# Performance work log

Hardware: AMD Instinct MI355X
Metric: run time of the kernel (lower is better)

The kernel has to match this reference:

```python
import jax, jax.numpy as jnp
import numpy as np
from jax import lax

H = 1024        # hidden_size
V_IN = 32000    # input_size (source vocab)
V_OUT = 32000   # output_size (target vocab)
S = 128         # source sentence length
MAX_STEPS = 51  # decode loop bound (loop <= 50)
EOS = 2         # target_vocab['<eos>']


def _lstm_cell(x, h, c, W_ih, W_hh, b_ih, b_hh):
    # torch LSTMCell: gate order i, f, g, o
    gates = jnp.dot(W_ih, x) + b_ih + jnp.dot(W_hh, h) + b_hh  # [4H]
    i, f, g, o = jnp.split(gates, 4)
    i = jax.nn.sigmoid(i)
    f = jax.nn.sigmoid(f)
    g = jnp.tanh(g)
    o = jax.nn.sigmoid(o)
    c2 = f * c + i * g
    return o * jnp.tanh(c2), c2


def setup_inputs() -> dict:
    key = jax.random.key(0)
    ks = jax.random.split(key, 16)
    sc = 0.02
    p = {}
    p['src_ids'] = jax.random.randint(ks[0], (S,), 1, V_IN)
    emb_in = jax.random.normal(ks[1], (V_IN, H), jnp.float32) * sc
    p['embed_input'] = emb_in.at[0].set(0.0)  # padding_idx=0
    p['W_ih_e'] = jax.random.normal(ks[2], (4 * H, H), jnp.float32) * sc
    p['W_hh_e'] = jax.random.normal(ks[3], (4 * H, H), jnp.float32) * sc
    p['b_ih_e'] = jnp.zeros((4 * H,), jnp.float32)
    p['b_hh_e'] = jnp.zeros((4 * H,), jnp.float32)
    p['W_li'] = jax.random.normal(ks[4], (V_OUT, H), jnp.float32) * sc
    p['b_li'] = jnp.zeros((V_OUT,), jnp.float32)
    emb_t = jax.random.normal(ks[5], (V_OUT, H), jnp.float32) * sc
    p['embed_target'] = emb_t.at[0].set(0.0)  # padding_idx=0
    p['W_ih_d'] = jax.random.normal(ks[6], (4 * H, H), jnp.float32) * sc
    p['W_hh_d'] = jax.random.normal(ks[7], (4 * H, H), jnp.float32) * sc
    p['b_ih_d'] = jnp.zeros((4 * H,), jnp.float32)
    p['b_hh_d'] = jnp.zeros((4 * H,), jnp.float32)
    p['W_lt'] = jax.random.normal(ks[8], (V_OUT, H), jnp.float32) * sc
    p['b_lt'] = jnp.zeros((V_OUT,), jnp.float32)
    p['W_tl'] = jax.random.normal(ks[9], (H, 2 * H), jnp.float32) * sc
    p['b_tl'] = jnp.zeros((H,), jnp.float32)
    return p


def reference(src_ids, embed_input, W_ih_e, W_hh_e, b_ih_e, b_hh_e,
              W_li, b_li, embed_target, W_ih_d, W_hh_d, b_ih_d, b_hh_d,
              W_lt, b_lt, W_tl, b_tl):
    # ---- encoder: sequential LSTMCell over source tokens ----
    def enc_step(carry, tok):
        h, c = carry
        x = embed_input[tok]
        h2, c2 = _lstm_cell(x, h, c, W_ih_e, W_hh_e, b_ih_e, b_hh_e)
        return (h2, c2), h2

    h0 = jnp.zeros((H,), embed_input.dtype)
    (hs, cx), hs_all = lax.scan(enc_step, (h0, h0), src_ids)  # hs_all: [S,H]

    # first predicted word from final encoder state (argmax(softmax(z)) == argmax(z))
    wid0 = jnp.argmax(jnp.dot(W_li, hs) + b_li)
    tk0 = embed_target[wid0]
    ht, cx = _lstm_cell(tk0, hs, cx, W_ih_d, W_hh_d, b_ih_d, b_hh_d)

    # ---- greedy decode loop (fixed 51 steps, masked after <eos>) ----
    def dec_step(carry, _):
        wid, ht, cx, done = carry
        target_k = embed_target[wid]
        # dot-product attention over encoder states, softmax along source dim
        scores = jnp.dot(hs_all, ht)              # [S]
        a_t = jax.nn.softmax(scores)              # [S]
        d = jnp.dot(a_t, hs_all)                  # [H]
        concat = jnp.concatenate([d, ht])         # [2H]
        ht_new = jnp.tanh(jnp.dot(W_tl, concat) + b_tl)
        logits = jnp.dot(W_lt, ht_new) + b_lt     # [V_OUT]
        wid_new = jnp.argmax(logits)
        is_eos = wid_new == EOS
        out_tok = jnp.where(done | is_eos, -1, wid_new)  # -1 = not emitted
        ht2, cx2 = _lstm_cell(target_k, ht, cx, W_ih_d, W_hh_d, b_ih_d, b_hh_d)
        return (wid_new, ht2, cx2, done | is_eos), (out_tok, logits)

    done0 = wid0 == EOS
    _, (toks, logits) = lax.scan(dec_step, (wid0, ht, cx, done0), None, length=MAX_STEPS)
    return toks, logits  # toks: [51] emitted ids (-1 after eos), logits: [51, V_OUT]
```

## Files before the change

kernel.cpp:

```cpp
#include <hip/hip_runtime.h>
#include <float.h>
#include <math.h>

#define H      1024
#define SLEN   128
#define VOUT   32000
#define NSTEP  51
#define EOS_ID 2
#define NB     256
#define BT     1024
#define NWAVES 16
#define HROWS  4
#define LROWS  125
#define TOKS_OFF 51
#define QTAB_BYTES (LROWS*H)

typedef float fv4 __attribute__((ext_vector_type(4)));

struct Xch {
  unsigned long long h [2][H];
  unsigned long long ht[2][H];
  unsigned long long sc[2][SLEN];
  unsigned long long pv[2][NB];
};
__device__ Xch g_x;

__device__ __forceinline__ float wredsum(float v){
  v += __shfl_xor(v, 32, 64);
  v += __shfl_xor(v, 16, 64);
  v += __shfl_xor(v,  8, 64);
  v += __shfl_xor(v,  4, 64);
  v += __shfl_xor(v,  2, 64);
  v += __shfl_xor(v,  1, 64);
  return v;
}
__device__ __forceinline__ float wredmax(float v){
  v = fmaxf(v, __shfl_xor(v, 32, 64));
  v = fmaxf(v, __shfl_xor(v, 16, 64));
  v = fmaxf(v, __shfl_xor(v,  8, 64));
  v = fmaxf(v, __shfl_xor(v,  4, 64));
  v = fmaxf(v, __shfl_xor(v,  2, 64));
  v = fmaxf(v, __shfl_xor(v,  1, 64));
  return v;
}
__device__ __forceinline__ float sigm(float x){ return 1.0f/(1.0f+expf(-x)); }

__device__ __forceinline__ unsigned long long pollraw(const unsigned long long* p, unsigned tag){
  unsigned long long v = __hip_atomic_load(p, __ATOMIC_RELAXED, __HIP_MEMORY_SCOPE_AGENT);
  while((unsigned)(v & 0xffull) != tag){
    __builtin_amdgcn_s_sleep(1);
    v = __hip_atomic_load(p, __ATOMIC_RELAXED, __HIP_MEMORY_SCOPE_AGENT);
  }
  return v;
}
__device__ __forceinline__ float pollf(const unsigned long long* p, unsigned tag){
  return __uint_as_float((unsigned)(pollraw(p, tag) >> 32));
}
__device__ __forceinline__ void pubf(unsigned long long* p, float x, unsigned tag){
  __hip_atomic_store(p, (((unsigned long long)__float_as_uint(x))<<32) | (unsigned long long)tag,
                     __ATOMIC_RELAXED, __HIP_MEMORY_SCOPE_AGENT);
}
__device__ __forceinline__ void pubpv(unsigned long long* p, float v, int idx, unsigned tag){
  unsigned long long lo = (((unsigned long long)(unsigned)idx) << 8) | (unsigned long long)tag;
  __hip_atomic_store(p, (((unsigned long long)__float_as_uint(v))<<32) | lo,
                     __ATOMIC_RELAXED, __HIP_MEMORY_SCOPE_AGENT);
}

__device__ __forceinline__ float partdot(const float* __restrict__ a,
                                         const float* __restrict__ hp, int lane){
  const float4* a4 = (const float4*)a;
  const float4* h4 = (const float4*)hp;
  float s = 0.f;
#pragma unroll
  for(int k=0;k<4;k++){
    float4 x = a4[lane + 64*k];
    float4 y = h4[lane + 64*k];
    s = fmaf(x.x,y.x,s); s = fmaf(x.y,y.y,s);
    s = fmaf(x.z,y.z,s); s = fmaf(x.w,y.w,s);
  }
  return s;
}
__device__ __forceinline__ float partdot_nt(const float* __restrict__ a,
                                            const float* __restrict__ hp, int lane){
  const fv4* a4 = (const fv4*)a;
  const float4* h4 = (const float4*)hp;
  float s = 0.f;
#pragma unroll
  for(int k=0;k<4;k++){
    fv4 x = __builtin_nontemporal_load(a4 + lane + 64*k);
    float4 y = h4[lane + 64*k];
    s = fmaf(x.x,y.x,s); s = fmaf(x.y,y.y,s);
    s = fmaf(x.z,y.z,s); s = fmaf(x.w,y.w,s);
  }
  return s;
}

__device__ __forceinline__ float dotq(unsigned u, float4 hv, float acc){
  acc = fmaf((float)((int)(u<<24)>>24), hv.x, acc);
  acc = fmaf((float)((int)(u<<16)>>24), hv.y, acc);
  acc = fmaf((float)((int)(u<< 8)>>24), hv.z, acc);
  acc = fmaf((float)((int) u     >>24), hv.w, acc);
  return acc;
}

extern "C" __global__ void __launch_bounds__(BT)
nmt_kernel(const int* __restrict__ src_ids,
           const float* __restrict__ embed_input,
           const float* __restrict__ W_ih_e, const float* __restrict__ W_hh_e,
           const float* __restrict__ b_ih_e, const float* __restrict__ b_hh_e,
           const float* __restrict__ W_li,  const float* __restrict__ b_li,
           const float* __restrict__ embed_target,
           const float* __restrict__ W_ih_d, const float* __restrict__ W_hh_d,
           const float* __restrict__ b_ih_d, const float* __restrict__ b_hh_d,
           const float* __restrict__ W_lt,  const float* __restrict__ b_lt,
           const float* __restrict__ W_tl,  const float* __restrict__ b_tl,
           float* __restrict__ out)
{
  const int tid  = threadIdx.x;
  const int b    = blockIdx.x;
  const int w    = tid >> 6;
  const int lane = tid & 63;
  const int grow = (w>>2)*H + 4*b + (w&3);

  extern __shared__ __align__(16) char qmem[];
  uint4* qtab = (uint4*)qmem;

  __shared__ __align__(16) float hbuf[H];
  __shared__ __align__(16) float hsrow[H];
  __shared__ __align__(16) float htn_lds[H];
  __shared__ __align__(16) float xenc[SLEN][NWAVES];
  __shared__ __align__(16) float Mloc[HROWS][SLEN];
  __shared__ __align__(16) float sraw[SLEN];
  __shared__ __align__(16) float vloc[128];
  __shared__ __align__(16) float qrho[128];
  __shared__ __align__(16) float qinv[128];
  __shared__ __align__(16) float qbias[128];
  __shared__ int   rlist[128];
  __shared__ float gw4[4][4];
  __shared__ float c4[4];
  __shared__ float hn2[NWAVES];
  __shared__ float wred2[4];
  __shared__ float redv[NWAVES];
  __shared__ int   redi[NWAVES];
  __shared__ float gwhh_l[NWAVES];
  __shared__ int   wid_sh, done_sh;
  __shared__ float e_sh, rhomax_sh;
  __shared__ int   rcnt_sh;

#define PVCOMBINE(TAG) do{                                                     \
    if(w<4){                                                                   \
      unsigned long long v = pollraw(&g_x.pv[(TAG)&1][(w<<6)+lane], (TAG));    \
      float val = __uint_as_float((unsigned)(v>>32));                          \
      int   idx = (int)((unsigned)(v>>8) & 0xffffffu);                         \
      _Pragma("unroll")                                                        \
      for(int dd=32; dd>=1; dd>>=1){                                           \
        float ov=__shfl_xor(val,dd,64); int oi=__shfl_xor(idx,dd,64);          \
        if(ov>val || (ov==val && oi<idx)){ val=ov; idx=oi; }                   \
      }                                                                        \
      if(lane==0){ redv[w]=val; redi[w]=idx; }                                 \
    }                                                                          \
    __syncthreads();                                                           \
  }while(0)

  hbuf[tid] = 0.f;
  if(tid<4) c4[tid] = 0.f;
  __syncthreads();

  {
    const float4* wr = (const float4*)(W_ih_e + (size_t)grow*H);
    float4 w0=wr[lane], w1=wr[lane+64], w2=wr[lane+128], w3=wr[lane+192];
    const float bias = b_ih_e[grow] + b_hh_e[grow];
    for(int t=0;t<SLEN;t++){
      const float4* xr = (const float4*)(embed_input + (size_t)src_ids[t]*H);
      float4 x0=xr[lane], x1=xr[lane+64], x2=xr[lane+128], x3=xr[lane+192];
      float s;
      s = w0.x*x0.x;        s = fmaf(w0.y,x0.y,s); s = fmaf(w0.z,x0.z,s); s = fmaf(w0.w,x0.w,s);
      s = fmaf(w1.x,x1.x,s); s = fmaf(w1.y,x1.y,s); s = fmaf(w1.z,x1.z,s); s = fmaf(w1.w,x1.w,s);
      s = fmaf(w2.x,x2.x,s); s = fmaf(w2.y,x2.y,s); s = fmaf(w2.z,x2.z,s); s = fmaf(w2.w,x2.w,s);
      s = fmaf(w3.x,x3.x,s); s = fmaf(w3.y,x3.y,s); s = fmaf(w3.w,x3.w,s); s = fmaf(w3.z,x3.z,s);
      s = wredsum(s);
      if(lane==0) xenc[t][w] = s + bias;
    }
  }
  __syncthreads();

  for(int t=0;t<SLEN;t++){
    {
      float s = wredsum(partdot(W_hh_e + (size_t)grow*H, hbuf, lane)) + xenc[t][w];
      if(lane==0) gw4[w>>2][w&3] = s;
    }
    __syncthreads();
    if(tid<4){
      float gi=gw4[0][tid], gf=gw4[1][tid], gg=gw4[2][tid], go=gw4[3][tid];
      float ii=sigm(gi), ff=sigm(gf), g2=tanhf(gg), oo=sigm(go);
      float c2=fmaf(ff, c4[tid], ii*g2);
      c4[tid]=c2;
      pubf(&g_x.h[(t+1)&1][4*b+tid], oo*tanhf(c2), (unsigned)(t+1));
    }
    hbuf[tid] = pollf(&g_x.h[(t+1)&1][tid], (unsigned)(t+1));
    __syncthreads();
    if(b==t) hsrow[tid]=hbuf[tid];
    if(w<HROWS){
      float s2 = wredsum(partdot(W_tl + (size_t)(4*b+w)*2*H, hbuf, lane));
      if(lane==0) Mloc[w][t]=s2;
    }
  }
  __syncthreads();

  {
    const int rbase = b*LROWS;
#pragma unroll
    for(int t=0;t<8;t++){
      const int j = w + NWAVES*t;
      if(j < LROWS){
        const fv4* wr = (const fv4*)(W_lt + (size_t)(rbase+j)*H);
        fv4 g0=__builtin_nontemporal_load(wr+4*lane);
        fv4 g1=__builtin_nontemporal_load(wr+4*lane+1);
        fv4 g2=__builtin_nontemporal_load(wr+4*lane+2);
        fv4 g3=__builtin_nontemporal_load(wr+4*lane+3);
        float4 f0={g0.x,g0.y,g0.z,g0.w}, f1={g1.x,g1.y,g1.z,g1.w};
        float4 f2={g2.x,g2.y,g2.z,g2.w}, f3={g3.x,g3.y,g3.z,g3.w};
        float m;
        m = fmaxf(fabsf(f0.x),fabsf(f0.y)); m=fmaxf(m,fmaxf(fabsf(f0.z),fabsf(f0.w)));
        m = fmaxf(m,fmaxf(fabsf(f1.x),fabsf(f1.y))); m=fmaxf(m,fmaxf(fabsf(f1.z),fabsf(f1.w)));
        m = fmaxf(m,fmaxf(fabsf(f2.x),fabsf(f2.y))); m=fmaxf(m,fmaxf(fabsf(f2.z),fabsf(f2.w)));
        m = fmaxf(m,fmaxf(fabsf(f3.x),fabsf(f3.y))); m=fmaxf(m,fmaxf(fabsf(f3.z),fabsf(f3.w)));
        m = wredmax(m);
        const float s    = (m>1e-30f) ? 127.0f/m : 0.f;
        const float invs = (m>1e-30f) ? m*(1.0f/127.0f) : 0.f;
        float rsq = 0.f;
        unsigned pk[4];
        float4 ff[4] = {f0,f1,f2,f3};
#pragma unroll
        for(int u=0;u<4;u++){
          int q0=(int)rintf(ff[u].x*s), q1=(int)rintf(ff[u].y*s);
          int q2=(int)rintf(ff[u].z*s), q3=(int)rintf(ff[u].w*s);
          float d0=ff[u].x-(float)q0*invs, d1=ff[u].y-(float)q1*invs;
          float d2=ff[u].z-(float)q2*invs, d3=ff[u].w-(float)q3*invs;
          rsq=fmaf(d0,d0,rsq); rsq=fmaf(d1,d1,rsq);
          rsq=fmaf(d2,d2,rsq); rsq=fmaf(d3,d3,rsq);
          pk[u] = ((unsigned)(q0&255)) | ((unsigned)(q1&255)<<8)
                | ((unsigned)(q2&255)<<16) | ((unsigned)(q3&255)<<24);
        }
        uint4 qq; qq.x=pk[0]; qq.y=pk[1]; qq.z=pk[2]; qq.w=pk[3];
        qtab[j*64 + lane] = qq;
        rsq = wredsum(rsq);
        if(lane==0){
          qrho[j]  = sqrtf(rsq)*1.0002f + 1e-8f;
          qinv[j]  = invs;
          qbias[j] = b_lt[rbase+j];
        }
      }
    }
  }
  __syncthreads();
  {
    float rv = (tid<LROWS) ? qrho[tid] : 0.f;
    if(tid<128){
      float m = wredmax(rv);
      if(lane==0) wred2[w]=m;
    }
  }
  __syncthreads();
  if(tid==0) rhomax_sh = fmaxf(wred2[0], wred2[1]);

  {
    float bestv=-FLT_MAX; int besti=0;
    for(int j=w; j<LROWS; j+=NWAVES){
      const int r = b*LROWS + j;
      float s = wredsum(partdot_nt(W_li + (size_t)r*H, hbuf, lane));
      if(lane==0){
        float v = s + b_li[r];
        if(v>bestv){ bestv=v; besti=r; }
      }
    }
    if(lane==0){ redv[w]=bestv; redi[w]=besti; }
    __syncthreads();
    if(tid==0){
      float bv=redv[0]; int bi=redi[0];
      for(int i=1;i<NWAVES;i++)
        if(redv[i]>bv || (redv[i]==bv && redi[i]<bi)){ bv=redv[i]; bi=redi[i]; }
      pubpv(&g_x.pv[1][b], bv, bi, 1u);
    }
  }
  PVCOMBINE(1u);
  if(tid==0){
    float bv=redv[0]; int bi=redi[0];
    for(int i=1;i<4;i++)
      if(redv[i]>bv || (redv[i]==bv && redi[i]<bi)){ bv=redv[i]; bi=redi[i]; }
    wid_sh = bi;
    done_sh = (bi==EOS_ID) ? 1 : 0;
  }
  __syncthreads();

  {
    const float* tk = embed_target + (size_t)wid_sh*H;
    float s = partdot(W_ih_d + (size_t)grow*H, tk, lane)
            + partdot(W_hh_d + (size_t)grow*H, hbuf, lane);
    s = wredsum(s);
    if(lane==0) gw4[w>>2][w&3] = s + b_ih_d[grow] + b_hh_d[grow];
  }
  __syncthreads();
  if(tid<4){
    float gi=gw4[0][tid], gf=gw4[1][tid], gg=gw4[2][tid], go=gw4[3][tid];
    float ii=sigm(gi), ff=sigm(gf), g2=tanhf(gg), oo=sigm(go);
    float c2=fmaf(ff, c4[tid], ii*g2);
    c4[tid]=c2;
    pubf(&g_x.h[1][4*b+tid], oo*tanhf(c2), 129u);
  }
  hbuf[tid] = pollf(&g_x.h[1][tid], 129u);
  __syncthreads();
  if(b<SLEN && w==0){
    float s = wredsum(partdot(hsrow, hbuf, lane));
    if(lane==0) pubf(&g_x.sc[1][b], s, 1u);
  }
  {
    float s=wredsum(partdot(W_hh_d + (size_t)grow*H, hbuf, lane));
    if(lane==0) gwhh_l[w]=s;
  }
  __syncthreads();

  for(int k=0;k<NSTEP;k++){
    const unsigned htag = (unsigned)(130+k);
    const unsigned ttag = (unsigned)(k+1);
    if(k>0){
      PVCOMBINE((unsigned)(k+1));
      if(tid==0){
        float bv=redv[0]; int bi=redi[0];
        for(int i=1;i<4;i++)
          if(redv[i]>bv || (redv[i]==bv && redi[i]<bi)){ bv=redv[i]; bi=redi[i]; }
        int iseos=(bi==EOS_ID)?1:0;
        if(b==0) out[k-1]=(float)((done_sh|iseos)?-1:bi);
        done_sh |= iseos;
        wid_sh = bi;
      }
      __syncthreads();
    }
    if(tid<SLEN) sraw[tid] = pollf(&g_x.sc[(k+1)&1][tid], (unsigned)(k+1));
    __syncthreads();
    if(tid<SLEN){
      float m = wredmax(sraw[tid]);
      if(lane==0) wred2[w]=m;
    }
    __syncthreads();
    if(tid<SLEN){
      float mx=fmaxf(wred2[0],wred2[1]);
      float e=expf(sraw[tid]-mx);
      sraw[tid]=e;
      float z=wredsum(e);
      if(lane==0) wred2[2+w]=z;
    }
    __syncthreads();
    {
      const float* tk=embed_target + (size_t)wid_sh*H;
      float s=wredsum(partdot(W_ih_d + (size_t)grow*H, tk, lane));
      if(lane==0) gw4[w>>2][w&3] = s + gwhh_l[w] + b_ih_d[grow] + b_hh_d[grow];
    }
    if(w<HROWS){
      const int r=4*b+w;
      float invZ=1.f/(wred2[2]+wred2[3]);
      float att=fmaf(sraw[2*lane],Mloc[w][2*lane], sraw[2*lane+1]*Mloc[w][2*lane+1]);
      float s=partdot(W_tl + (size_t)r*2*H + H, hbuf, lane);
      float tot=wredsum(fmaf(att,invZ,s));
      if(lane==0) pubf(&g_x.ht[ttag&1][r], tanhf(tot + b_tl[r]), ttag);
    }
    __syncthreads();
    if(tid<4){
      float gi=gw4[0][tid], gf=gw4[1][tid], gg=gw4[2][tid], go=gw4[3][tid];
      float ii=sigm(gi), ff=sigm(gf), g2=tanhf(gg), oo=sigm(go);
      float c2=fmaf(ff, c4[tid], ii*g2);
      c4[tid]=c2;
      pubf(&g_x.h[htag&1][4*b+tid], oo*tanhf(c2), htag);
    }
    htn_lds[tid] = pollf(&g_x.ht[ttag&1][tid], ttag);
    hbuf[tid]    = pollf(&g_x.h [htag&1][tid], htag);
    __syncthreads();
    {
      float x = htn_lds[tid];
      float ss = wredsum(x*x);
      if(lane==0) hn2[w]=ss;
      if(tid==0) rcnt_sh=0;
    }
    __syncthreads();
    if(tid==0){
      float t2=0.f;
      for(int i=0;i<NWAVES;i++) t2+=hn2[i];
      float e = rhomax_sh * sqrtf(t2) * 1.0002f + 2e-3f;
      if(!(e>0.f && e<1e6f)) e=3.0e38f;
      e_sh = e;
    }
    {
      const float4* h4=(const float4*)htn_lds;
      float4 h0=h4[4*lane], h1=h4[4*lane+1], h2=h4[4*lane+2], h3=h4[4*lane+3];
#pragma unroll
      for(int t=0;t<8;t++){
        const int j=w+NWAVES*t;
        if(j<LROWS){
          uint4 q = qtab[j*64 + lane];
          float acc=0.f;
          acc=dotq(q.x,h0,acc); acc=dotq(q.y,h1,acc);
          acc=dotq(q.z,h2,acc); acc=dotq(q.w,h3,acc);
          acc=wredsum(acc);
          if(lane==0) vloc[j] = acc*qinv[j] + qbias[j];
        }
      }
    }
    __syncthreads();
    {
      const size_t obase = TOKS_OFF + (size_t)k*VOUT + (size_t)b*LROWS;
      if(tid<LROWS) out[obase+tid]=vloc[tid];
      float mv=(tid<LROWS)?vloc[tid]:-FLT_MAX;
      if(tid<128){
        float m=wredmax(mv);
        if(lane==0) wred2[w]=m;
      }
    }
    __syncthreads();
    {
      float thr = fmaxf(wred2[0],wred2[1]) - 2.0f*e_sh;
      if(tid<LROWS && vloc[tid]>=thr){
        int pos=atomicAdd(&rcnt_sh,1);
        rlist[pos]=tid;
      }
    }
    __syncthreads();
    {
      float bestv=-FLT_MAX; int besti=0x7fffffff;
      const int nr=rcnt_sh;
      for(int s2=w;s2<nr;s2+=NWAVES){
        const int r=b*LROWS+rlist[s2];
        float s=wredsum(partdot_nt(W_lt + (size_t)r*H, htn_lds, lane));
        if(lane==0){
          float f=s+qbias[rlist[s2]];
          if(f>bestv || (f==bestv && r<besti)){ bestv=f; besti=r; }
        }
      }
      if(lane==0){ redv[w]=bestv; redi[w]=besti; }
    }
    if(b<SLEN && w==0){
      float s=wredsum(partdot(hsrow, hbuf, lane));
      if(lane==0) pubf(&g_x.sc[(k+2)&1][b], s, (unsigned)(k+2));
    }
    {
      float s=wredsum(partdot(W_hh_d + (size_t)grow*H, hbuf, lane));
      if(lane==0) gwhh_l[w]=s;
    }
    __syncthreads();
    if(tid==0){
      float bv=redv[0]; int bi=redi[0];
      for(int i=1;i<NWAVES;i++)
        if(redv[i]>bv || (redv[i]==bv && redi[i]<bi)){ bv=redv[i]; bi=redi[i]; }
      pubpv(&g_x.pv[(k+2)&1][b], bv, bi, (unsigned)(k+2));
    }
  }

  if(b==0){
    PVCOMBINE((unsigned)(NSTEP+1));
    if(tid==0){
      float bv=redv[0]; int bi=redi[0];
      for(int i=1;i<4;i++)
        if(redv[i]>bv || (redv[i]==bv && redi[i]<bi)){ bv=redv[i]; bi=redi[i]; }
      int iseos=(bi==EOS_ID)?1:0;
      out[NSTEP-1]=(float)((done_sh|iseos)?-1:bi);
    }
  }
#undef PVCOMBINE
}

extern "C" void kernel_launch(void* const* d_in, const int* in_sizes, int n_in,
                              void* d_out, int out_size, void* d_ws, size_t ws_size,
                              hipStream_t stream) {
  const int*   src_ids      = (const int*)  d_in[0];
  const float* embed_input  = (const float*)d_in[1];
  const float* W_ih_e       = (const float*)d_in[2];
  const float* W_hh_e       = (const float*)d_in[3];
  const float* b_ih_e       = (const float*)d_in[4];
  const float* b_hh_e       = (const float*)d_in[5];
  const float* W_li         = (const float*)d_in[6];
  const float* b_li         = (const float*)d_in[7];
  const float* embed_target = (const float*)d_in[8];
  const float* W_ih_d       = (const float*)d_in[9];
  const float* W_hh_d       = (const float*)d_in[10];
  const float* b_ih_d       = (const float*)d_in[11];
  const float* b_hh_d       = (const float*)d_in[12];
  const float* W_lt         = (const float*)d_in[13];
  const float* b_lt         = (const float*)d_in[14];
  const float* W_tl         = (const float*)d_in[15];
  const float* b_tl         = (const float*)d_in[16];
  float*       out          = (float*)d_out;

  void* sptr = nullptr;
  (void)hipGetSymbolAddress(&sptr, HIP_SYMBOL(g_x));
  if(sptr) (void)hipMemsetAsync(sptr, 0, sizeof(Xch), stream);

  void* args[] = {
    (void*)&src_ids, (void*)&embed_input,
    (void*)&W_ih_e, (void*)&W_hh_e, (void*)&b_ih_e, (void*)&b_hh_e,
    (void*)&W_li, (void*)&b_li, (void*)&embed_target,
    (void*)&W_ih_d, (void*)&W_hh_d, (void*)&b_ih_d, (void*)&b_hh_d,
    (void*)&W_lt, (void*)&b_lt, (void*)&W_tl, (void*)&b_tl,
    (void*)&out
  };

  hipError_t err = hipLaunchCooperativeKernel((const void*)nmt_kernel,
                                              dim3(NB), dim3(BT), args,
                                              QTAB_BYTES, stream);
  if (err != hipSuccess) {
    nmt_kernel<<<dim3(NB), dim3(BT), QTAB_BYTES, stream>>>(
        src_ids, embed_input, W_ih_e, W_hh_e, b_ih_e, b_hh_e,
        W_li, b_li, embed_target, W_ih_d, W_hh_d, b_ih_d, b_hh_d,
        W_lt, b_lt, W_tl, b_tl, out);
  }
}
```

Baseline: 2.420 ms.

## Reorder decode step so argmax poll overlaps attention and h poll moves late

Reorders the per-step schedule of the persistent decode kernel. The attention/W_tl output projection is now computed before the cross-block argmax combine, and waves 4-7 poll the argmax partials so they do not collide with waves 0-3 doing attention. The hidden-state poll and the score/W_hh products move to the end of the step, after the vocab-logit pass, so the inter-block wait overlaps other work. The encoder input projection is also unrolled by two tokens to expose more memory parallelism. This adds extra barriers and changes the dependency order, so ordering mistakes could introduce stalls or races.

```diff
diff --git a/kernel.cpp b/kernel.cpp
--- a/kernel.cpp
+++ b/kernel.cpp
@@ -147,9 +147,9 @@
   __shared__ float e_sh, rhomax_sh;
   __shared__ int   rcnt_sh;
 
-#define PVCOMBINE(TAG) do{                                                     \
-    if(w<4){                                                                   \
-      unsigned long long v = pollraw(&g_x.pv[(TAG)&1][(w<<6)+lane], (TAG));    \
+#define PVPOLL47(TAG) do{                                                      \
+    if(w>=4 && w<8){                                                           \
+      unsigned long long v = pollraw(&g_x.pv[(TAG)&1][((w-4)<<6)+lane], (TAG));\
       float val = __uint_as_float((unsigned)(v>>32));                          \
       int   idx = (int)((unsigned)(v>>8) & 0xffffffu);                         \
       _Pragma("unroll")                                                        \
@@ -159,7 +159,6 @@
       }                                                                        \
       if(lane==0){ redv[w]=val; redi[w]=idx; }                                 \
     }                                                                          \
-    __syncthreads();                                                           \
   }while(0)
 
   hbuf[tid] = 0.f;
@@ -170,16 +169,22 @@
     const float4* wr = (const float4*)(W_ih_e + (size_t)grow*H);
     float4 w0=wr[lane], w1=wr[lane+64], w2=wr[lane+128], w3=wr[lane+192];
     const float bias = b_ih_e[grow] + b_hh_e[grow];
-    for(int t=0;t<SLEN;t++){
+    for(int t=0;t<SLEN;t+=2){
       const float4* xr = (const float4*)(embed_input + (size_t)src_ids[t]*H);
+      const float4* yr = (const float4*)(embed_input + (size_t)src_ids[t+1]*H);
       float4 x0=xr[lane], x1=xr[lane+64], x2=xr[lane+128], x3=xr[lane+192];
-      float s;
+      float4 y0=yr[lane], y1=yr[lane+64], y2=yr[lane+128], y3=yr[lane+192];
+      float s, u;
       s = w0.x*x0.x;        s = fmaf(w0.y,x0.y,s); s = fmaf(w0.z,x0.z,s); s = fmaf(w0.w,x0.w,s);
+      u = w0.x*y0.x;        u = fmaf(w0.y,y0.y,u); u = fmaf(w0.z,y0.z,u); u = fmaf(w0.w,y0.w,u);
       s = fmaf(w1.x,x1.x,s); s = fmaf(w1.y,x1.y,s); s = fmaf(w1.z,x1.z,s); s = fmaf(w1.w,x1.w,s);
+      u = fmaf(w1.x,y1.x,u); u = fmaf(w1.y,y1.y,u); u = fmaf(w1.z,y1.z,u); u = fmaf(w1.w,y1.w,u);
       s = fmaf(w2.x,x2.x,s); s = fmaf(w2.y,x2.y,s); s = fmaf(w2.z,x2.z,s); s = fmaf(w2.w,x2.w,s);
+      u = fmaf(w2.x,y2.x,u); u = fmaf(w2.y,y2.y,u); u = fmaf(w2.z,y2.z,u); u = fmaf(w2.w,y2.w,u);
       s = fmaf(w3.x,x3.x,s); s = fmaf(w3.y,x3.y,s); s = fmaf(w3.w,x3.w,s); s = fmaf(w3.z,x3.z,s);
-      s = wredsum(s);
-      if(lane==0) xenc[t][w] = s + bias;
+      u = fmaf(w3.x,y3.x,u); u = fmaf(w3.y,y3.y,u); u = fmaf(w3.w,y3.w,u); u = fmaf(w3.z,y3.z,u);
+      s = wredsum(s); u = wredsum(u);
+      if(lane==0){ xenc[t][w] = s + bias; xenc[t+1][w] = u + bias; }
     }
   }
   __syncthreads();
@@ -283,10 +288,12 @@
       pubpv(&g_x.pv[1][b], bv, bi, 1u);
     }
   }
-  PVCOMBINE(1u);
+  __syncthreads();
+  PVPOLL47(1u);
+  __syncthreads();
   if(tid==0){
-    float bv=redv[0]; int bi=redi[0];
-    for(int i=1;i<4;i++)
+    float bv=redv[4]; int bi=redi[4];
+    for(int i=5;i<8;i++)
       if(redv[i]>bv || (redv[i]==bv && redi[i]<bi)){ bv=redv[i]; bi=redi[i]; }
     wid_sh = bi;
     done_sh = (bi==EOS_ID) ? 1 : 0;
@@ -323,20 +330,7 @@
   for(int k=0;k<NSTEP;k++){
     const unsigned htag = (unsigned)(130+k);
     const unsigned ttag = (unsigned)(k+1);
-    if(k>0){
-      PVCOMBINE((unsigned)(k+1));
-      if(tid==0){
-        float bv=redv[0]; int bi=redi[0];
-        for(int i=1;i<4;i++)
-          if(redv[i]>bv || (redv[i]==bv && redi[i]<bi)){ bv=redv[i]; bi=redi[i]; }
-        int iseos=(bi==EOS_ID)?1:0;
-        if(b==0) out[k-1]=(float)((done_sh|iseos)?-1:bi);
-        done_sh |= iseos;
-        wid_sh = bi;
-      }
-      __syncthreads();
-    }
-    if(tid<SLEN) sraw[tid] = pollf(&g_x.sc[(k+1)&1][tid], (unsigned)(k+1));
+    if(tid<SLEN) sraw[tid] = pollf(&g_x.sc[ttag&1][tid], ttag);
     __syncthreads();
     if(tid<SLEN){
       float m = wredmax(sraw[tid]);
@@ -351,11 +345,6 @@
       if(lane==0) wred2[2+w]=z;
     }
     __syncthreads();
-    {
-      const float* tk=embed_target + (size_t)wid_sh*H;
-      float s=wredsum(partdot(W_ih_d + (size_t)grow*H, tk, lane));
-      if(lane==0) gw4[w>>2][w&3] = s + gwhh_l[w] + b_ih_d[grow] + b_hh_d[grow];
-    }
     if(w<HROWS){
       const int r=4*b+w;
       float invZ=1.f/(wred2[2]+wred2[3]);
@@ -364,6 +353,23 @@
       float tot=wredsum(fmaf(att,invZ,s));
       if(lane==0) pubf(&g_x.ht[ttag&1][r], tanhf(tot + b_tl[r]), ttag);
     }
+    if(k>0) PVPOLL47(ttag);
+    __syncthreads();
+    if(k>0 && tid==0){
+      float bv=redv[4]; int bi=redi[4];
+      for(int i=5;i<8;i++)
+        if(redv[i]>bv || (redv[i]==bv && redi[i]<bi)){ bv=redv[i]; bi=redi[i]; }
+      int iseos=(bi==EOS_ID)?1:0;
+      if(b==0) out[k-1]=(float)((done_sh|iseos)?-1:bi);
+      done_sh |= iseos;
+      wid_sh = bi;
+    }
+    __syncthreads();
+    {
+      const float* tk=embed_target + (size_t)wid_sh*H;
+      float s=wredsum(partdot(W_ih_d + (size_t)grow*H, tk, lane));
+      if(lane==0) gw4[w>>2][w&3] = s + gwhh_l[w] + b_ih_d[grow] + b_hh_d[grow];
+    }
     __syncthreads();
     if(tid<4){
       float gi=gw4[0][tid], gf=gw4[1][tid], gg=gw4[2][tid], go=gw4[3][tid];
@@ -373,7 +379,6 @@
       pubf(&g_x.h[htag&1][4*b+tid], oo*tanhf(c2), htag);
     }
     htn_lds[tid] = pollf(&g_x.ht[ttag&1][tid], ttag);
-    hbuf[tid]    = pollf(&g_x.h [htag&1][tid], htag);
     __syncthreads();
     {
       float x = htn_lds[tid];
@@ -437,14 +442,6 @@
       }
       if(lane==0){ redv[w]=bestv; redi[w]=besti; }
     }
-    if(b<SLEN && w==0){
-      float s=wredsum(partdot(hsrow, hbuf, lane));
-      if(lane==0) pubf(&g_x.sc[(k+2)&1][b], s, (unsigned)(k+2));
-    }
-    {
-      float s=wredsum(partdot(W_hh_d + (size_t)grow*H, hbuf, lane));
-      if(lane==0) gwhh_l[w]=s;
-    }
     __syncthreads();
     if(tid==0){
       float bv=redv[0]; int bi=redi[0];
@@ -452,19 +449,31 @@
         if(redv[i]>bv || (redv[i]==bv && redi[i]<bi)){ bv=redv[i]; bi=redi[i]; }
       pubpv(&g_x.pv[(k+2)&1][b], bv, bi, (unsigned)(k+2));
     }
+    hbuf[tid] = pollf(&g_x.h[htag&1][tid], htag);
+    __syncthreads();
+    if(b<SLEN && w==0){
+      float s=wredsum(partdot(hsrow, hbuf, lane));
+      if(lane==0) pubf(&g_x.sc[(k+2)&1][b], s, (unsigned)(k+2));
+    }
+    {
+      float s=wredsum(partdot(W_hh_d + (size_t)grow*H, hbuf, lane));
+      if(lane==0) gwhh_l[w]=s;
+    }
+    __syncthreads();
   }
 
   if(b==0){
-    PVCOMBINE((unsigned)(NSTEP+1));
+    PVPOLL47((unsigned)(NSTEP+1));
+    __syncthreads();
     if(tid==0){
-      float bv=redv[0]; int bi=redi[0];
-      for(int i=1;i<4;i++)
+      float bv=redv[4]; int bi=redi[4];
+      for(int i=5;i<8;i++)
         if(redv[i]>bv || (redv[i]==bv && redi[i]<bi)){ bv=redv[i]; bi=redi[i]; }
       int iseos=(bi==EOS_ID)?1:0;
       out[NSTEP-1]=(float)((done_sh|iseos)?-1:bi);
     }
   }
-#undef PVCOMBINE
+#undef PVPOLL47
 }
 
 extern "C" void kernel_launch(void* const* d_in, const int* in_sizes, int n_in,
```

New measurement: 2.272 ms. 1.07x faster.
